# Performance work log

Measured on AMD Instinct MI355X. Metric: run time of the kernel, lower is better.

## Reference

```python
import jax, jax.numpy as jnp
import numpy as np

N = [40000, 10000, 2500, 625, 157]  # vertex counts per mesh level (0 = full res)
K = 6


def _propagate(x, row, col, norm, n):
    # x: [B, N_in, C]; gather neighbor feats, weight by norm, scatter-add to rows
    msg = x[:, col, :] * norm[None, :, None]          # [B, E, C]
    return jnp.zeros((x.shape[0], n, x.shape[2]), x.dtype).at[:, row, :].add(msg)


def cheb_conv(x, edge_index, W, b, n):
    # Chebyshev graph conv with sym-normalized adjacency (lambda_max=2 / CoMA convention)
    row, col = edge_index[0], edge_index[1]
    deg = jnp.zeros((n,), x.dtype).at[row].add(jnp.ones(row.shape, x.dtype))
    dinv = jnp.where(deg > 0, deg ** -0.5, jnp.zeros_like(deg))
    norm = dinv[row] * dinv[col]
    Tx0 = x
    out = jnp.einsum('bnc,cd->bnd', Tx0, W[0])
    Tx1 = _propagate(Tx0, row, col, norm, n)
    out = out + jnp.einsum('bnc,cd->bnd', Tx1, W[1])
    for k in range(2, W.shape[0]):
        Tx2 = 2.0 * _propagate(Tx1, row, col, norm, n) - Tx0
        out = out + jnp.einsum('bnc,cd->bnd', Tx2, W[k])
        Tx0, Tx1 = Tx1, Tx2
    return out + b


def pool(x, row, col, val, n_out):
    # sparse COO upsampling: out[:, row] += val * x[:, col]  (Pool() in torch source)
    msg = x[:, col, :] * val[None, :, None]
    return jnp.zeros((x.shape[0], n_out, x.shape[2]), x.dtype).at[:, row, :].add(msg)


def setup_inputs() -> dict:
    key = jax.random.key(0)
    ks = iter(jax.random.split(key, 64))
    B, latent = 16, 128
    inp = {}
    inp['x'] = jax.random.normal(next(ks), (B, latent), jnp.float32)
    inp['lin_w'] = jax.random.normal(next(ks), (latent, N[4] * 64), jnp.float32) * 0.05
    inp['lin_b'] = jnp.zeros((N[4] * 64,), jnp.float32)
    for i in range(4):
        inp[f'edge{i}'] = jax.random.randint(next(ks), (2, 6 * N[i]), 0, N[i])
    for i in range(4):
        nnz = 3 * N[i]
        inp[f'up{i}_row'] = jax.random.randint(next(ks), (nnz,), 0, N[i])
        inp[f'up{i}_col'] = jax.random.randint(next(ks), (nnz,), 0, N[i + 1])
        inp[f'up{i}_val'] = jax.random.uniform(next(ks), (nnz,), jnp.float32)
    # Deblock Cheb weights: (in,out) = (64,64),(64,32),(32,32),(32,32); final (32,3)
    for j, (ci, co) in enumerate([(64, 64), (64, 32), (32, 32), (32, 32)], start=1):
        inp[f'W{j}'] = jax.random.normal(next(ks), (K, ci, co), jnp.float32) * 0.05
        inp[f'b{j}'] = jnp.zeros((co,), jnp.float32)
    inp['Wout'] = jax.random.normal(next(ks), (K, 32, 3), jnp.float32) * 0.05
    inp['bout'] = jnp.zeros((3,), jnp.float32)
    return inp


def reference(x, lin_w, lin_b, edge0, edge1, edge2, edge3,
              up0_row, up0_col, up0_val, up1_row, up1_col, up1_val,
              up2_row, up2_col, up2_val, up3_row, up3_col, up3_val,
              W1, b1, W2, b2, W3, b3, W4, b4, Wout, bout):
    B = x.shape[0]
    h = (x @ lin_w + lin_b).reshape(B, N[4], 64)        # latent -> coarsest mesh
    edges = [edge0, edge1, edge2, edge3]
    ups = [(up0_row, up0_col, up0_val), (up1_row, up1_col, up1_val),
           (up2_row, up2_col, up2_val), (up3_row, up3_col, up3_val)]
    Ws = [(W1, b1), (W2, b2), (W3, b3), (W4, b4)]
    for j in range(4):
        lvl = 3 - j  # deblock j upsamples to mesh level lvl (coarse -> fine)
        row, col, val = ups[lvl]
        h = pool(h, row, col, val, N[lvl])
        h = jax.nn.elu(cheb_conv(h, edges[lvl], Ws[j][0], Ws[j][1], N[lvl]))
    return cheb_conv(h, edge0, Wout, bout, N[0])        # [B, 40000, 3]
```

## Files before the change

### kernel.cpp

```cpp
#include <hip/hip_runtime.h>
#include <math.h>

#define TB 256
#define SCAN_TOT 106250
#define SCAN_NB  104

typedef __bf16 bf16x8 __attribute__((ext_vector_type(8)));
typedef float f32x4 __attribute__((ext_vector_type(4)));

static __device__ __forceinline__ int gtid() { return blockIdx.x * blockDim.x + threadIdx.x; }

static __device__ __forceinline__ void fma4(float4& a, float s, const float4 b) {
  a.x = fmaf(s, b.x, a.x); a.y = fmaf(s, b.y, a.y);
  a.z = fmaf(s, b.z, a.z); a.w = fmaf(s, b.w, a.w);
}

static __device__ __forceinline__ float bf_lo(unsigned u) {
  union { unsigned u; float f; } c; c.u = u << 16; return c.f;
}
static __device__ __forceinline__ float bf_hi(unsigned u) {
  union { unsigned u; float f; } c; c.u = u & 0xffff0000u; return c.f;
}
static __device__ __forceinline__ float bfus(unsigned short u) {
  union { unsigned u; float f; } c; c.u = ((unsigned)u) << 16; return c.f;
}
static __device__ __forceinline__ unsigned f2bf(float f) {
  union { float f; unsigned u; } c; c.f = f;
  return (c.u + 0x7fffu + ((c.u >> 16) & 1u)) >> 16;
}
static __device__ __forceinline__ unsigned pk2(float a, float b) {
  return f2bf(a) | (f2bf(b) << 16);
}

__global__ void fill_kernel(float* __restrict__ p, int n, float v) {
  int i = gtid(); if (i < n) p[i] = v;
}

__global__ void zero_int_kernel(int* __restrict__ p, int n) {
  int i = gtid(); if (i < n) p[i] = 0;
}

struct SegD {
  const int* rows[8];
  const int* cols[8];
  const float* vals[8];
  int start[8];
  int degb[8];
};

__global__ void count_all_kernel(SegD sg, int total, int* __restrict__ deg) {
  int t = gtid(); if (t >= total) return;
  int seg = 0;
  #pragma unroll
  for (int q = 1; q < 8; ++q) seg += (t >= sg.start[q]);
  int i = t - sg.start[seg];
  atomicAdd(&deg[sg.degb[seg] + sg.rows[seg][i]], 1);
}

__global__ void fill_all_kernel(SegD sg, int total, const int* __restrict__ deg,
                                const int* __restrict__ offs, int* __restrict__ cursor,
                                int* __restrict__ ccol, float* __restrict__ cwa) {
  int t = gtid(); if (t >= total) return;
  int seg = 0;
  #pragma unroll
  for (int q = 1; q < 8; ++q) seg += (t >= sg.start[q]);
  int i = t - sg.start[seg];
  int db = sg.degb[seg];
  int r = sg.rows[seg][i];
  int c = sg.cols[seg][i];
  int p = atomicAdd(&cursor[db + r], 1);
  int idx = offs[db + r] + p;
  float w;
  if (sg.vals[seg]) {
    w = sg.vals[seg][i];
  } else {
    int dc = deg[db + c];
    w = rsqrtf((float)deg[db + r]) * (dc > 0 ? rsqrtf((float)dc) : 0.f);
  }
  ccol[idx] = c;
  cwa[idx] = w;
}

__global__ void scan_phase1(const int* __restrict__ in, int* __restrict__ bsum) {
  __shared__ int wsum[4];
  int blk = blockIdx.x, t = threadIdx.x;
  int base = blk * 1024 + t * 4;
  int s = 0;
  #pragma unroll
  for (int q = 0; q < 4; ++q) { int i = base + q; if (i < SCAN_TOT) s += in[i]; }
  #pragma unroll
  for (int o = 32; o > 0; o >>= 1) s += __shfl_xor(s, o, 64);
  int lane = t & 63, wid = t >> 6;
  if (lane == 0) wsum[wid] = s;
  __syncthreads();
  if (t == 0) bsum[blk] = wsum[0] + wsum[1] + wsum[2] + wsum[3];
}

__global__ void scan_phase2(int* __restrict__ bsum, int* __restrict__ offs_end) {
  int t = threadIdx.x;
  int v = (t < SCAN_NB) ? bsum[t] : 0;
  int lane = t & 63, wid = t >> 6;
  int p = v;
  #pragma unroll
  for (int o = 1; o < 64; o <<= 1) { int u = __shfl_up(p, o, 64); if (lane >= o) p += u; }
  __shared__ int w0tot;
  if (wid == 0 && lane == 63) w0tot = p;
  __syncthreads();
  int incl = p + (wid ? w0tot : 0);
  if (t < SCAN_NB) bsum[t] = incl - v;
  if (t == 127) offs_end[0] = incl;
}

__global__ void scan_phase3(const int* __restrict__ in, const int* __restrict__ bbase,
                            int* __restrict__ offs, int* __restrict__ cursor) {
  __shared__ int wsum[4];
  int blk = blockIdx.x, t = threadIdx.x;
  int base = blk * 1024 + t * 4;
  int v[4]; int s = 0;
  #pragma unroll
  for (int q = 0; q < 4; ++q) { int i = base + q; v[q] = (i < SCAN_TOT) ? in[i] : 0; s += v[q]; }
  int lane = t & 63, wid = t >> 6;
  int p = s;
  #pragma unroll
  for (int o = 1; o < 64; o <<= 1) { int u = __shfl_up(p, o, 64); if (lane >= o) p += u; }
  if (lane == 63) wsum[wid] = p;
  __syncthreads();
  int woff = 0;
  #pragma unroll
  for (int q = 0; q < 4; ++q) woff += (q < wid) ? wsum[q] : 0;
  int ex = bbase[blk] + woff + p - s;
  #pragma unroll
  for (int q = 0; q < 4; ++q) {
    int i = base + q;
    if (i < SCAN_TOT) { offs[i] = ex; cursor[i] = 0; ex += v[q]; }
  }
}

__global__ void pool_kernel(const float4* __restrict__ x, const int* __restrict__ offs,
                            const int* __restrict__ ccol, const float* __restrict__ cw,
                            float4* __restrict__ out, int n, int xs4, int xoff4,
                            int os4, int osh) {
  int t = gtid();
  if (t >= n * os4) return;
  int v = t >> osh, j = t & (os4 - 1);
  int s = offs[v], e = offs[v + 1];
  float4 a = {0.f, 0.f, 0.f, 0.f};
  for (int i = s; i < e; ++i)
    fma4(a, cw[i], x[(long long)ccol[i] * xs4 + xoff4 + j]);
  out[t] = a;
}

__global__ void pool0_bf16_kernel(const float4* __restrict__ x, const int* __restrict__ offs,
                                  const int* __restrict__ ccol, const float* __restrict__ cw,
                                  uint4* __restrict__ out, int n) {
  int t = gtid();
  if (t >= n * 64) return;
  int v = t >> 6, j = t & 63;
  int s = offs[v], e = offs[v + 1];
  float4 a0 = {0.f, 0.f, 0.f, 0.f}, a1 = {0.f, 0.f, 0.f, 0.f};
  for (int i = s; i < e; ++i) {
    float w = cw[i];
    const float4* xr = x + (long long)ccol[i] * 128 + j * 2;
    fma4(a0, w, xr[0]); fma4(a1, w, xr[1]);
  }
  uint4 r;
  r.x = pk2(a0.x, a0.y); r.y = pk2(a0.z, a0.w);
  r.z = pk2(a1.x, a1.y); r.w = pk2(a1.z, a1.w);
  out[t] = r;
}

template<int CIN, int COUT>
__global__ void cheb_step_kernel(const float* __restrict__ X,
                                 const float* __restrict__ b1,
                                 float* __restrict__ b2o,
                                 const float* __restrict__ Wk,
                                 const float* __restrict__ bias,
                                 const int* __restrict__ offs,
                                 const int* __restrict__ ccol,
                                 const float* __restrict__ cw,
                                 int n, int LB, int mode) {
  constexpr int CS = COUT / 8;
  constexpr int LCS = (CS == 8) ? 3 : 2;
  constexpr int W4 = COUT / 4;
  __shared__ float sW[CIN * COUT];
  for (int i = threadIdx.x; i < CIN * COUT; i += blockDim.x) sW[i] = Wk[i];
  __syncthreads();
  int t = gtid();
  int BI = 1 << LB;
  if (t >= n * BI * CS) return;
  int cs = t & (CS - 1);
  int r = t >> LCS;
  int v = r >> LB;
  int bi = r & (BI - 1);
  float4 a0 = {0.f, 0.f, 0.f, 0.f}, a1 = {0.f, 0.f, 0.f, 0.f};
  const float4* Xr = (const float4*)(X + (long long)r * CIN);
  const float4* wbase = ((const float4*)sW) + cs * 2;
  #pragma unroll
  for (int c4 = 0; c4 < CIN / 4; ++c4) {
    float4 xv = Xr[c4];
    const float4* w = wbase + (c4 * 4) * W4;
    fma4(a0, xv.x, w[0]); fma4(a1, xv.x, w[1]); w += W4;
    fma4(a0, xv.y, w[0]); fma4(a1, xv.y, w[1]); w += W4;
    fma4(a0, xv.z, w[0]); fma4(a1, xv.z, w[1]); w += W4;
    fma4(a0, xv.w, w[0]); fma4(a1, xv.w, w[1]);
  }
  if (mode >= 1) {
    float sc = (mode == 3) ? 1.f : 2.f;
    int s = offs[v], e = offs[v + 1];
    const float4* b14 = (const float4*)b1;
    for (int i = s; i < e; ++i) {
      float w = cw[i] * sc;
      long long rb = (long long)((ccol[i] << LB) | bi) * W4 + cs * 2;
      fma4(a0, w, b14[rb]); fma4(a1, w, b14[rb + 1]);
    }
  }
  float4* Or = ((float4*)b2o) + (long long)r * W4 + cs * 2;
  if (mode >= 2) {
    float4 p0 = Or[0], p1 = Or[1];
    a0.x -= p0.x; a0.y -= p0.y; a0.z -= p0.z; a0.w -= p0.w;
    a1.x -= p1.x; a1.y -= p1.y; a1.z -= p1.z; a1.w -= p1.w;
  }
  if (mode == 3) {
    const float* bs = bias + cs * 8;
    a0.x += bs[0]; a0.y += bs[1]; a0.z += bs[2]; a0.w += bs[3];
    a1.x += bs[4]; a1.y += bs[5]; a1.z += bs[6]; a1.w += bs[7];
    a0.x = a0.x > 0.f ? a0.x : expm1f(a0.x);
    a0.y = a0.y > 0.f ? a0.y : expm1f(a0.y);
    a0.z = a0.z > 0.f ? a0.z : expm1f(a0.z);
    a0.w = a0.w > 0.f ? a0.w : expm1f(a0.w);
    a1.x = a1.x > 0.f ? a1.x : expm1f(a1.x);
    a1.y = a1.y > 0.f ? a1.y : expm1f(a1.y);
    a1.z = a1.z > 0.f ? a1.z : expm1f(a1.z);
    a1.w = a1.w > 0.f ? a1.w : expm1f(a1.w);
  }
  Or[0] = a0; Or[1] = a1;
}

__global__ void __launch_bounds__(256)
cheb0_mfma_kernel(const uint4* __restrict__ X,
                  const unsigned short* __restrict__ b1,
                  unsigned short* __restrict__ b2o,
                  const float* __restrict__ Wk,
                  const float* __restrict__ bias,
                  const int* __restrict__ offs,
                  const int* __restrict__ ccol,
                  const float* __restrict__ cw,
                  int n, int mode) {
  int lane = threadIdx.x & 63;
  int v = (blockIdx.x << 2) | (threadIdx.x >> 6);
  if (v >= n) return;
  int g = lane >> 4;
  int c15 = lane & 15;

  union { uint4 u; bf16x8 v; } Au;
  Au.u = X[((long long)(v * 16 + c15)) * 4 + g];

  bf16x8 B0, B1;
  #pragma unroll
  for (int j = 0; j < 8; ++j) {
    int k = 8 * g + j;
    B0[j] = (__bf16)Wk[k * 32 + c15];
    B1[j] = (__bf16)Wk[k * 32 + 16 + c15];
  }
  f32x4 z = {0.f, 0.f, 0.f, 0.f};
  f32x4 acc0 = __builtin_amdgcn_mfma_f32_16x16x32_bf16(Au.v, B0, z, 0, 0, 0);
  f32x4 acc1 = __builtin_amdgcn_mfma_f32_16x16x32_bf16(Au.v, B1, z, 0, 0, 0);

  if (mode >= 1) {
    float sc = (mode == 3) ? 1.f : 2.f;
    int s = offs[v], e = offs[v + 1];
    for (int i = s; i < e; ++i) {
      float w = cw[i] * sc;
      long long base = ((long long)ccol[i] * 16 + 4 * g) * 32;
      #pragma unroll
      for (int q = 0; q < 4; ++q) {
        acc0[q] = fmaf(w, bfus(b1[base + q * 32 + c15]), acc0[q]);
        acc1[q] = fmaf(w, bfus(b1[base + q * 32 + 16 + c15]), acc1[q]);
      }
    }
  }
  long long rb = ((long long)v * 16 + 4 * g) * 32;
  if (mode >= 2) {
    #pragma unroll
    for (int q = 0; q < 4; ++q) {
      acc0[q] -= bfus(b2o[rb + q * 32 + c15]);
      acc1[q] -= bfus(b2o[rb + q * 32 + 16 + c15]);
    }
  }
  if (mode == 3) {
    float bs0 = bias[c15], bs1 = bias[16 + c15];
    #pragma unroll
    for (int q = 0; q < 4; ++q) {
      float a = acc0[q] + bs0;
      float b = acc1[q] + bs1;
      acc0[q] = a > 0.f ? a : expm1f(a);
      acc1[q] = b > 0.f ? b : expm1f(b);
    }
  }
  #pragma unroll
  for (int q = 0; q < 4; ++q) {
    b2o[rb + q * 32 + c15] = (unsigned short)f2bf(acc0[q]);
    b2o[rb + q * 32 + 16 + c15] = (unsigned short)f2bf(acc1[q]);
  }
}

__global__ void gemm_out_all_kernel(const uint4* __restrict__ X, const float* __restrict__ W,
                                    unsigned short* __restrict__ c_all, int nr) {
  __shared__ float sW[576];
  for (int i = threadIdx.x; i < 576; i += blockDim.x) sW[i] = W[i];
  __syncthreads();
  int r = gtid();
  if (r >= nr) return;
  const uint4* Xr = X + (long long)r * 4;
  float xa[32];
  #pragma unroll
  for (int q = 0; q < 4; ++q) {
    uint4 xv = Xr[q];
    xa[q * 8 + 0] = bf_lo(xv.x); xa[q * 8 + 1] = bf_hi(xv.x);
    xa[q * 8 + 2] = bf_lo(xv.y); xa[q * 8 + 3] = bf_hi(xv.y);
    xa[q * 8 + 4] = bf_lo(xv.z); xa[q * 8 + 5] = bf_hi(xv.z);
    xa[q * 8 + 6] = bf_lo(xv.w); xa[q * 8 + 7] = bf_hi(xv.w);
  }
  float acc[18];
  #pragma unroll
  for (int i = 0; i < 18; ++i) acc[i] = 0.f;
  #pragma unroll
  for (int c = 0; c < 32; ++c) {
    float xc = xa[c];
    #pragma unroll
    for (int k = 0; k < 6; ++k) {
      acc[k * 3 + 0] = fmaf(xc, sW[k * 96 + c * 3 + 0], acc[k * 3 + 0]);
      acc[k * 3 + 1] = fmaf(xc, sW[k * 96 + c * 3 + 1], acc[k * 3 + 1]);
      acc[k * 3 + 2] = fmaf(xc, sW[k * 96 + c * 3 + 2], acc[k * 3 + 2]);
    }
  }
  #pragma unroll
  for (int k = 0; k < 6; ++k) {
    unsigned short* o = c_all + ((long long)k * nr + r) * 3;
    o[0] = (unsigned short)f2bf(acc[k * 3 + 0]);
    o[1] = (unsigned short)f2bf(acc[k * 3 + 1]);
    o[2] = (unsigned short)f2bf(acc[k * 3 + 2]);
  }
}

__global__ void cheb_out_step_kernel(const unsigned short* __restrict__ c_all, int k,
                                     const float* __restrict__ b1,
                                     float* __restrict__ b2o,
                                     const float* __restrict__ bias,
                                     const int* __restrict__ offs,
                                     const int* __restrict__ ccol,
                                     const float* __restrict__ cw,
                                     int n, float* __restrict__ dout, int mode) {
  int r = gtid();
  if (r >= n * 16) return;
  int v = r >> 4, bi = r & 15;
  const unsigned short* cr = c_all + ((long long)k * n * 16 + r) * 3;
  float a0 = bfus(cr[0]), a1 = bfus(cr[1]), a2 = bfus(cr[2]);
  if (mode >= 1) {
    float sc = (mode == 3) ? 1.f : 2.f;
    int s = offs[v], e = offs[v + 1];
    for (int i = s; i < e; ++i) {
      float w = cw[i] * sc;
      const float* br = b1 + (long long)((ccol[i] << 4) | bi) * 3;
      a0 = fmaf(w, br[0], a0); a1 = fmaf(w, br[1], a1); a2 = fmaf(w, br[2], a2);
    }
  }
  if (mode >= 2) {
    const float* p = b2o + (long long)r * 3;
    a0 -= p[0]; a1 -= p[1]; a2 -= p[2];
  }
  if (mode == 3) {
    a0 += bias[0]; a1 += bias[1]; a2 += bias[2];
    float* o = dout + ((long long)bi * n + v) * 3;
    o[0] = a0; o[1] = a1; o[2] = a2;
  } else {
    float* o = b2o + (long long)r * 3;
    o[0] = a0; o[1] = a1; o[2] = a2;
  }
}

__global__ void linear_kernel(const float* __restrict__ x, const float* __restrict__ w,
                              const float* __restrict__ bias, float* __restrict__ out) {
  int t = gtid();
  const int TOT = 157 * 16 * 64;
  if (t >= TOT) return;
  int c = t & 63;
  int b = (t >> 6) & 15;
  int v = t >> 10;
  int colw = v * 64 + c;
  float acc = bias[colw];
  const float* xr = x + b * 128;
  for (int k = 0; k < 128; ++k) acc = fmaf(xr[k], w[k * 10048 + colw], acc);
  out[t] = acc;
}

extern "C" void kernel_launch(void* const* d_in, const int* in_sizes, int n_in,
                              void* d_out, int out_size, void* d_ws, size_t ws_size,
                              hipStream_t stream) {
  const int N[4] = {40000, 10000, 2500, 625};
  const int E[4] = {240000, 60000, 15000, 3750};
  const int NNZ[4] = {120000, 30000, 7500, 1875};
  const int DP[4] = {0, 40000, 50000, 52500};
  const int DE[4] = {53125, 93125, 103125, 105625};
  const int ITEMS = 478125;

  const float* x     = (const float*)d_in[0];
  const float* lin_w = (const float*)d_in[1];
  const float* lin_b = (const float*)d_in[2];
  const int* edge[4] = {(const int*)d_in[3], (const int*)d_in[4], (const int*)d_in[5], (const int*)d_in[6]};
  const int* up_row[4]; const int* up_col[4]; const float* up_val[4];
  for (int i = 0; i < 4; ++i) {
    up_row[i] = (const int*)d_in[7 + 3 * i];
    up_col[i] = (const int*)d_in[8 + 3 * i];
    up_val[i] = (const float*)d_in[9 + 3 * i];
  }
  const float* W_[5] = {(const float*)d_in[19], (const float*)d_in[21], (const float*)d_in[23],
                        (const float*)d_in[25], (const float*)d_in[27]};
  const float* b_[5] = {(const float*)d_in[20], (const float*)d_in[22], (const float*)d_in[24],
                        (const float*)d_in[26], (const float*)d_in[28]};

  char* ws = (char*)d_ws;
  size_t off = 0;
  auto alloc = [&](size_t bytes) -> void* {
    void* p = ws + off;
    off = (off + bytes + 255) & ~(size_t)255;
    return p;
  };
  auto cdiv = [](int a, int b) { return (a + b - 1) / b; };

  float* slot[4];
  for (int i = 0; i < 4; ++i) slot[i] = (float*)alloc(20480000ull);
  uint4* Ab = (uint4*)alloc(40960000ull);
  uint4* Bb = (uint4*)alloc(40960000ull);
  uint4* Cb = (uint4*)alloc(40960000ull);
  unsigned short* c_all = (unsigned short*)alloc((size_t)6 * 640000 * 3 * 2);
  float* ob1 = (float*)alloc((size_t)640000 * 3 * 4);
  float* ob2 = (float*)alloc((size_t)640000 * 3 * 4);
  int* deg_all    = (int*)alloc(SCAN_TOT * 4);
  int* cursor_all = (int*)alloc(SCAN_TOT * 4);
  int* offs_all   = (int*)alloc((SCAN_TOT + 1) * 4);
  int* bsum       = (int*)alloc(SCAN_NB * 4);
  int* col_arena  = (int*)alloc((size_t)ITEMS * 4);
  float* w_arena  = (float*)alloc((size_t)ITEMS * 4);

  if (off > ws_size) {
    fill_kernel<<<cdiv(out_size, TB), TB, 0, stream>>>((float*)d_out, out_size,
                                                       (float)(ws_size >> 20));
    return;
  }

  SegD sg;
  int cum = 0;
  for (int l = 0; l < 4; ++l) {
    sg.rows[l] = up_row[l]; sg.cols[l] = up_col[l]; sg.vals[l] = up_val[l];
    sg.start[l] = cum; sg.degb[l] = DP[l]; cum += NNZ[l];
  }
  for (int l = 0; l < 4; ++l) {
    sg.rows[4 + l] = edge[l]; sg.cols[4 + l] = edge[l] + E[l]; sg.vals[4 + l] = nullptr;
    sg.start[4 + l] = cum; sg.degb[4 + l] = DE[l]; cum += E[l];
  }
  zero_int_kernel<<<cdiv(SCAN_TOT, TB), TB, 0, stream>>>(deg_all, SCAN_TOT);
  count_all_kernel<<<cdiv(ITEMS, TB), TB, 0, stream>>>(sg, ITEMS, deg_all);
  scan_phase1<<<SCAN_NB, TB, 0, stream>>>(deg_all, bsum);
  scan_phase2<<<1, 128, 0, stream>>>(bsum, offs_all + SCAN_TOT);
  scan_phase3<<<SCAN_NB, TB, 0, stream>>>(deg_all, bsum, offs_all, cursor_all);
  fill_all_kernel<<<cdiv(ITEMS, TB), TB, 0, stream>>>(sg, ITEMS, deg_all, offs_all,
                                                      cursor_all, col_arena, w_arena);

  linear_kernel<<<cdiv(157 * 16 * 64, TB), TB, 0, stream>>>(x, lin_w, lin_b, slot[0]);
  float* H = slot[0];
  float* A = slot[1];
  float* B = slot[2];
  float* C = slot[3];

  const int CINA[3]  = {64, 64, 32};
  const int COUTA[3] = {64, 32, 32};

  for (int j = 0; j < 3; ++j) {
    int lvl = 3 - j;
    int n = N[lvl];
    int cin = CINA[j], cout = COUTA[j];
    int os4 = 16 * cin / 4;
    int osh = (os4 == 256) ? 8 : 7;
    const int* offs_p = offs_all + DP[lvl];
    const int* offs_e = offs_all + DE[lvl];

    pool_kernel<<<cdiv(n * os4, TB), TB, 0, stream>>>(
        (const float4*)H, offs_p, col_arena, w_arena, (float4*)A, n, os4, 0, os4, osh);

    int cs = cout / 8;
    dim3 g(cdiv(n * 16 * cs, TB));
    auto step = [&](const float* b1, float* b2o, int k, int mode) {
      const float* Wk = W_[j] + (size_t)k * cin * cout;
      if (cin == 64 && cout == 64)
        hipLaunchKernelGGL((cheb_step_kernel<64, 64>), g, dim3(TB), 0, stream,
                           A, b1, b2o, Wk, b_[j], offs_e, col_arena, w_arena, n, 4, mode);
      else if (cin == 64 && cout == 32)
        hipLaunchKernelGGL((cheb_step_kernel<64, 32>), g, dim3(TB), 0, stream,
                           A, b1, b2o, Wk, b_[j], offs_e, col_arena, w_arena, n, 4, mode);
      else
        hipLaunchKernelGGL((cheb_step_kernel<32, 32>), g, dim3(TB), 0, stream,
                           A, b1, b2o, Wk, b_[j], offs_e, col_arena, w_arena, n, 4, mode);
    };
    step(nullptr, B, 5, 0);
    step(B, C, 4, 1);
    step(C, B, 3, 2);
    step(B, C, 2, 2);
    step(C, B, 1, 2);
    step(B, C, 0, 3);

    float* tmp = H; H = C; C = tmp;
  }

  {
    int n = N[0];
    int nr = n * 16;
    const int* offs_p = offs_all + DP[0];
    const int* offs_e = offs_all + DE[0];
    dim3 g64(cdiv(n * 64, TB));
    dim3 gmf(n / 4);
    dim3 gr(cdiv(nr, TB));

    pool0_bf16_kernel<<<g64, dim3(TB), 0, stream>>>(
        (const float4*)H, offs_p, col_arena, w_arena, Ab, n);

    auto dstep = [&](const uint4* b1, uint4* b2o, int k, int mode) {
      cheb0_mfma_kernel<<<gmf, dim3(TB), 0, stream>>>(
          Ab, (const unsigned short*)b1, (unsigned short*)b2o,
          W_[3] + (size_t)k * 1024, b_[3],
          offs_e, col_arena, w_arena, n, mode);
    };
    dstep(nullptr, Bb, 5, 0);
    dstep(Bb, Cb, 4, 1);
    dstep(Cb, Bb, 3, 2);
    dstep(Bb, Cb, 2, 2);
    dstep(Cb, Bb, 1, 2);
    dstep(Bb, Cb, 0, 3);

    gemm_out_all_kernel<<<gr, dim3(TB), 0, stream>>>(Cb, W_[4], c_all, nr);
    float* dout = (float*)d_out;
    auto ostep = [&](const float* b1, float* b2o, int k, int mode) {
      cheb_out_step_kernel<<<gr, dim3(TB), 0, stream>>>(
          c_all, k, b1, b2o, b_[4], offs_e, col_arena, w_arena, n, dout, mode);
    };
    ostep(nullptr, ob1, 5, 0);
    ostep(ob1, ob2, 4, 1);
    ostep(ob2, ob1, 3, 2);
    ostep(ob1, ob2, 2, 2);
    ostep(ob2, ob1, 1, 2);
    ostep(ob1, ob2, 0, 3);
  }
}
```

Before: 856.7 us.

## Use bf16 MFMA Chebyshev kernel for level-1 deblock and pack intermediates

The third deblock (level 1, 32->32 channels, 10000 vertices) now runs through the bf16 MFMA Chebyshev kernel instead of the fp32 scalar step kernel. The level-0 pool then reads bf16 input directly. The intermediate Chebyshev buffers are stored as packed 32-bit pairs of bf16 so each lane does one 32-bit load or store instead of two 16-bit accesses. The final ELU output keeps the original bf16 row layout. The aim is to cut memory traffic and ALU work on level 1, at the cost of bf16 precision at that level.

```diff
diff --git a/kernel.cpp b/kernel.cpp
--- a/kernel.cpp
+++ b/kernel.cpp
@@ -150,9 +150,9 @@
   out[t] = a;
 }
 
-__global__ void pool0_bf16_kernel(const float4* __restrict__ x, const int* __restrict__ offs,
-                                  const int* __restrict__ ccol, const float* __restrict__ cw,
-                                  uint4* __restrict__ out, int n) {
+__global__ void pool_f2b_kernel(const float4* __restrict__ x, const int* __restrict__ offs,
+                                const int* __restrict__ ccol, const float* __restrict__ cw,
+                                uint4* __restrict__ out, int n) {
   int t = gtid();
   if (t >= n * 64) return;
   int v = t >> 6, j = t & 63;
@@ -166,6 +166,30 @@
   uint4 r;
   r.x = pk2(a0.x, a0.y); r.y = pk2(a0.z, a0.w);
   r.z = pk2(a1.x, a1.y); r.w = pk2(a1.z, a1.w);
+  out[t] = r;
+}
+
+__global__ void pool_b2b_kernel(const uint4* __restrict__ x, const int* __restrict__ offs,
+                                const int* __restrict__ ccol, const float* __restrict__ cw,
+                                uint4* __restrict__ out, int n) {
+  int t = gtid();
+  if (t >= n * 64) return;
+  int v = t >> 6, j = t & 63;
+  int s = offs[v], e = offs[v + 1];
+  float a[8];
+  #pragma unroll
+  for (int q = 0; q < 8; ++q) a[q] = 0.f;
+  for (int i = s; i < e; ++i) {
+    float w = cw[i];
+    uint4 xv = x[(long long)ccol[i] * 64 + j];
+    a[0] = fmaf(w, bf_lo(xv.x), a[0]); a[1] = fmaf(w, bf_hi(xv.x), a[1]);
+    a[2] = fmaf(w, bf_lo(xv.y), a[2]); a[3] = fmaf(w, bf_hi(xv.y), a[3]);
+    a[4] = fmaf(w, bf_lo(xv.z), a[4]); a[5] = fmaf(w, bf_hi(xv.z), a[5]);
+    a[6] = fmaf(w, bf_lo(xv.w), a[6]); a[7] = fmaf(w, bf_hi(xv.w), a[7]);
+  }
+  uint4 r;
+  r.x = pk2(a[0], a[1]); r.y = pk2(a[2], a[3]);
+  r.z = pk2(a[4], a[5]); r.w = pk2(a[6], a[7]);
   out[t] = r;
 }
 
@@ -237,15 +261,15 @@
 }
 
 __global__ void __launch_bounds__(256)
-cheb0_mfma_kernel(const uint4* __restrict__ X,
-                  const unsigned short* __restrict__ b1,
-                  unsigned short* __restrict__ b2o,
-                  const float* __restrict__ Wk,
-                  const float* __restrict__ bias,
-                  const int* __restrict__ offs,
-                  const int* __restrict__ ccol,
-                  const float* __restrict__ cw,
-                  int n, int mode) {
+cheb_mfma32_kernel(const uint4* __restrict__ X,
+                   const unsigned* __restrict__ b1,
+                   unsigned* __restrict__ b2o,
+                   const float* __restrict__ Wk,
+                   const float* __restrict__ bias,
+                   const int* __restrict__ offs,
+                   const int* __restrict__ ccol,
+                   const float* __restrict__ cw,
+                   int n, int mode) {
   int lane = threadIdx.x & 63;
   int v = (blockIdx.x << 2) | (threadIdx.x >> 6);
   if (v >= n) return;
@@ -271,36 +295,41 @@
     int s = offs[v], e = offs[v + 1];
     for (int i = s; i < e; ++i) {
       float w = cw[i] * sc;
-      long long base = ((long long)ccol[i] * 16 + 4 * g) * 32;
+      long long base = (long long)ccol[i] * 256 + 64 * g + c15;
       #pragma unroll
       for (int q = 0; q < 4; ++q) {
-        acc0[q] = fmaf(w, bfus(b1[base + q * 32 + c15]), acc0[q]);
-        acc1[q] = fmaf(w, bfus(b1[base + q * 32 + 16 + c15]), acc1[q]);
+        unsigned pv = b1[base + 16 * q];
+        acc0[q] = fmaf(w, bf_lo(pv), acc0[q]);
+        acc1[q] = fmaf(w, bf_hi(pv), acc1[q]);
       }
     }
   }
-  long long rb = ((long long)v * 16 + 4 * g) * 32;
+  long long rb = (long long)v * 256 + 64 * g + c15;
   if (mode >= 2) {
     #pragma unroll
     for (int q = 0; q < 4; ++q) {
-      acc0[q] -= bfus(b2o[rb + q * 32 + c15]);
-      acc1[q] -= bfus(b2o[rb + q * 32 + 16 + c15]);
+      unsigned pv = b2o[rb + 16 * q];
+      acc0[q] -= bf_lo(pv);
+      acc1[q] -= bf_hi(pv);
     }
   }
   if (mode == 3) {
     float bs0 = bias[c15], bs1 = bias[16 + c15];
+    unsigned short* o = (unsigned short*)b2o;
+    long long lb = ((long long)v * 16 + 4 * g) * 32;
     #pragma unroll
     for (int q = 0; q < 4; ++q) {
       float a = acc0[q] + bs0;
       float b = acc1[q] + bs1;
-      acc0[q] = a > 0.f ? a : expm1f(a);
-      acc1[q] = b > 0.f ? b : expm1f(b);
+      a = a > 0.f ? a : expm1f(a);
+      b = b > 0.f ? b : expm1f(b);
+      o[lb + q * 32 + c15] = (unsigned short)f2bf(a);
+      o[lb + q * 32 + 16 + c15] = (unsigned short)f2bf(b);
     }
-  }
-  #pragma unroll
-  for (int q = 0; q < 4; ++q) {
-    b2o[rb + q * 32 + c15] = (unsigned short)f2bf(acc0[q]);
-    b2o[rb + q * 32 + 16 + c15] = (unsigned short)f2bf(acc1[q]);
+  } else {
+    #pragma unroll
+    for (int q = 0; q < 4; ++q)
+      b2o[rb + 16 * q] = pk2(acc0[q], acc1[q]);
   }
 }
 
@@ -431,8 +460,8 @@
   float* slot[4];
   for (int i = 0; i < 4; ++i) slot[i] = (float*)alloc(20480000ull);
   uint4* Ab = (uint4*)alloc(40960000ull);
-  uint4* Bb = (uint4*)alloc(40960000ull);
-  uint4* Cb = (uint4*)alloc(40960000ull);
+  unsigned* Bb = (unsigned*)alloc(40960000ull);
+  unsigned* Cb = (unsigned*)alloc(40960000ull);
   unsigned short* c_all = (unsigned short*)alloc((size_t)6 * 640000 * 3 * 2);
   float* ob1 = (float*)alloc((size_t)640000 * 3 * 4);
   float* ob2 = (float*)alloc((size_t)640000 * 3 * 4);
@@ -473,10 +502,10 @@
   float* B = slot[2];
   float* C = slot[3];
 
-  const int CINA[3]  = {64, 64, 32};
-  const int COUTA[3] = {64, 32, 32};
-
-  for (int j = 0; j < 3; ++j) {
+  const int CINA[2]  = {64, 64};
+  const int COUTA[2] = {64, 32};
+
+  for (int j = 0; j < 2; ++j) {
     int lvl = 3 - j;
     int n = N[lvl];
     int cin = CINA[j], cout = COUTA[j];
@@ -495,11 +524,8 @@
       if (cin == 64 && cout == 64)
         hipLaunchKernelGGL((cheb_step_kernel<64, 64>), g, dim3(TB), 0, stream,
                            A, b1, b2o, Wk, b_[j], offs_e, col_arena, w_arena, n, 4, mode);
-      else if (cin == 64 && cout == 32)
+      else
         hipLaunchKernelGGL((cheb_step_kernel<64, 32>), g, dim3(TB), 0, stream,
-                           A, b1, b2o, Wk, b_[j], offs_e, col_arena, w_arena, n, 4, mode);
-      else
-        hipLaunchKernelGGL((cheb_step_kernel<32, 32>), g, dim3(TB), 0, stream,
                            A, b1, b2o, Wk, b_[j], offs_e, col_arena, w_arena, n, 4, mode);
     };
     step(nullptr, B, 5, 0);
@@ -511,23 +537,46 @@
 
     float* tmp = H; H = C; C = tmp;
   }
+  float* freeA = A;
+  float* freeB = B;
+  float* freeC = C;
+
+  uint4* Ab1 = (uint4*)freeA;
+  unsigned* Bb1 = (unsigned*)freeB;
+  unsigned* Cb1 = (unsigned*)freeC;
+  {
+    int n = N[1];
+    const int* offs_p = offs_all + DP[1];
+    const int* offs_e = offs_all + DE[1];
+    pool_f2b_kernel<<<cdiv(n * 64, TB), TB, 0, stream>>>(
+        (const float4*)H, offs_p, col_arena, w_arena, Ab1, n);
+    dim3 gmf(n / 4);
+    auto dstep = [&](const unsigned* b1, unsigned* b2o, int k, int mode) {
+      cheb_mfma32_kernel<<<gmf, dim3(TB), 0, stream>>>(
+          Ab1, b1, b2o, W_[2] + (size_t)k * 1024, b_[2],
+          offs_e, col_arena, w_arena, n, mode);
+    };
+    dstep(nullptr, Bb1, 5, 0);
+    dstep(Bb1, Cb1, 4, 1);
+    dstep(Cb1, Bb1, 3, 2);
+    dstep(Bb1, Cb1, 2, 2);
+    dstep(Cb1, Bb1, 1, 2);
+    dstep(Bb1, Cb1, 0, 3);
+  }
 
   {
     int n = N[0];
     int nr = n * 16;
     const int* offs_p = offs_all + DP[0];
     const int* offs_e = offs_all + DE[0];
-    dim3 g64(cdiv(n * 64, TB));
+
+    pool_b2b_kernel<<<cdiv(n * 64, TB), TB, 0, stream>>>(
+        (const uint4*)Cb1, offs_p, col_arena, w_arena, Ab, n);
+
     dim3 gmf(n / 4);
-    dim3 gr(cdiv(nr, TB));
-
-    pool0_bf16_kernel<<<g64, dim3(TB), 0, stream>>>(
-        (const float4*)H, offs_p, col_arena, w_arena, Ab, n);
-
-    auto dstep = [&](const uint4* b1, uint4* b2o, int k, int mode) {
-      cheb0_mfma_kernel<<<gmf, dim3(TB), 0, stream>>>(
-          Ab, (const unsigned short*)b1, (unsigned short*)b2o,
-          W_[3] + (size_t)k * 1024, b_[3],
+    auto dstep = [&](const unsigned* b1, unsigned* b2o, int k, int mode) {
+      cheb_mfma32_kernel<<<gmf, dim3(TB), 0, stream>>>(
+          Ab, b1, b2o, W_[3] + (size_t)k * 1024, b_[3],
           offs_e, col_arena, w_arena, n, mode);
     };
     dstep(nullptr, Bb, 5, 0);
@@ -537,7 +586,8 @@
     dstep(Cb, Bb, 1, 2);
     dstep(Bb, Cb, 0, 3);
 
-    gemm_out_all_kernel<<<gr, dim3(TB), 0, stream>>>(Cb, W_[4], c_all, nr);
+    dim3 gr(cdiv(nr, TB));
+    gemm_out_all_kernel<<<gr, dim3(TB), 0, stream>>>((const uint4*)Cb, W_[4], c_all, nr);
     float* dout = (float*)d_out;
     auto ostep = [&](const float* b1, float* b2o, int k, int mode) {
       cheb_out_step_kernel<<<gr, dim3(TB), 0, stream>>>(
```

Result: faster. 761.4 us (-11.1%).
